# Kernel optimization log

Hardware: AMD Instinct MI355X
Metric: run time of the kernel (lower is better)

Reference implementation:

```python
import jax, jax.numpy as jnp
import numpy as np

A_COEF = 4e-4
B_COEF = 2e-2
T = 0.5
ATT = 1.0


def setup_inputs() -> dict:
    key = jax.random.key(0)
    k1, k2, k3, k4 = jax.random.split(key, 4)
    return {
        "targets": jnp.zeros((1,), dtype=jnp.int32),
        "stu1": jax.random.normal(k1, (8, 256, 64, 64), dtype=jnp.float32),
        "tea1": jax.random.normal(k2, (8, 256, 64, 64), dtype=jnp.float32),
        "stu2": jax.random.normal(k3, (8, 512, 32, 32), dtype=jnp.float32),
        "tea2": jax.random.normal(k4, (8, 512, 32, 32), dtype=jnp.float32),
    }


def _level_terms(s, t):
    # s, t: [B, C, H, W]
    BS, C, H, W = s.shape
    HW = H * W
    # spatial attention maps [B,H,W] and channel attention maps [B,C]
    Gs_s = jnp.abs(s).sum(axis=1) / C
    Gs_t = jnp.abs(t).sum(axis=1) / C
    Gc_s = jnp.abs(s).sum(axis=(2, 3)) / HW
    Gc_t = jnp.abs(t).sum(axis=(2, 3)) / HW
    # sum-reduction MSE between attention maps
    lat = jnp.sum((Gs_s - Gs_t) ** 2) + jnp.sum((Gc_s - Gc_t) ** 2)
    # spatial softmax mask over flattened HW (matches per-batch exp/max/sum loop)
    Ms = HW * jax.nn.softmax(((Gs_s + Gs_t) / T).reshape(BS, HW), axis=1).reshape(BS, H, W)
    # channel softmax mask
    Mc = C * jax.nn.softmax((Gc_s + Gc_t) / T, axis=1)
    # slam = sum_{b,c} Mc[b,c] * sum_{h,w} (s-t)^2 * Ms[b,h,w]
    slam = jnp.einsum('bchw,bhw,bc->', (s - t) ** 2, Ms, Mc)
    return lat, jnp.sqrt(slam)


def reference(targets, stu1, tea1, stu2, tea2):
    levels = ((stu1, tea1), (stu2, tea2))
    lat = jnp.float32(0.0)
    lam = jnp.float32(0.0)
    BS = stu1.shape[0]
    for s, t in levels:
        l_at, l_am = _level_terms(s, t)
        lat = lat + l_at
        lam = lam + l_am
    att_loss = ATT * (A_COEF * lat + B_COEF * lam) / BS / len(levels)
    return (att_loss * BS, jax.lax.stop_gradient(att_loss)[None])
```

## Files before the change

kernel.cpp:

```cpp
#include <hip/hip_runtime.h>
#include <hip/hip_fp16.h>
#include <math.h>

#define B_   8
#define C1   256
#define HW1  4096
#define C2   512
#define HW2  1024

#define CCH  8
#define HWT  1024
#define NCH1 32
#define NCH2 64
#define NT1  4
#define NT2  1

#define NB1  (B_*NT1*NCH1)
#define NB2  (B_*NCH2)
#define NBS  (NB1+NB2)

#define F_LATP  0
#define F_SL1P  (F_LATP + 32)
#define F_SL2P  (F_SL1P + NB1)
#define F_CP1S  (F_SL2P + NB2)
#define F_CP1T  (F_CP1S + B_*C1*NT1)
#define F_CP2S  (F_CP1T + B_*C1*NT1)
#define F_CP2T  (F_CP2S + B_*C2)
#define F_GS1S  (F_CP2T + B_*C2)
#define F_GS1T  (F_GS1S + B_*HW1)
#define F_GS2S  (F_GS1T + B_*HW1)
#define F_GS2T  (F_GS2S + B_*HW2)
#define F_MS1   (F_GS2T + B_*HW2)
#define F_MC1   (F_MS1 + B_*HW1)
#define F_MS2   (F_MC1 + B_*C1)
#define F_MC2   (F_MS2 + B_*HW2)
#define F_APH   (F_MC2 + B_*C2)
#define NH1     (NCH1*B_*HW1)
#define NH2     (NCH2*B_*HW2)
#define APH_FLOATS ((2*NH1 + 2*NH2) / 2)
#define F_D8    (F_APH + APH_FLOATS)
#define ND1     (B_*C1*HW1)
#define ND2     (B_*C2*HW2)

struct alignas(8) h4 { __half2 a, b; };
typedef float v2f __attribute__((ext_vector_type(2)));

__device__ __forceinline__ float wave_reduce_sum(float v) {
#pragma unroll
    for (int off = 1; off < 64; off <<= 1) v += __shfl_xor(v, off, 64);
    return v;
}
__device__ __forceinline__ float wave_reduce_max(float v) {
#pragma unroll
    for (int off = 1; off < 64; off <<= 1) v = fmaxf(v, __shfl_xor(v, off, 64));
    return v;
}
__device__ __forceinline__ float block_reduce_sum(float v, float* red) {
    const int lane = threadIdx.x & 63, wid = threadIdx.x >> 6;
    v = wave_reduce_sum(v);
    if (lane == 0) red[wid] = v;
    __syncthreads();
    v = red[0] + red[1] + red[2] + red[3];
    __syncthreads();
    return v;
}
__device__ __forceinline__ float block_reduce_max(float v, float* red) {
    const int lane = threadIdx.x & 63, wid = threadIdx.x >> 6;
    v = wave_reduce_max(v);
    if (lane == 0) red[wid] = v;
    __syncthreads();
    v = fmaxf(fmaxf(red[0], red[1]), fmaxf(red[2], red[3]));
    __syncthreads();
    return v;
}

__device__ __forceinline__ unsigned int pack4_fp8(float q0, float q1, float q2, float q3) {
    int u = 0;
    u = __builtin_amdgcn_cvt_pk_fp8_f32(q0, q1, u, false);
    u = __builtin_amdgcn_cvt_pk_fp8_f32(q2, q3, u, true);
    return (unsigned int)u;
}

template<int C, int HW, int NT>
__device__ void stats_level(const float* __restrict__ s, const float* __restrict__ t,
                            __half* __restrict__ APs, __half* __restrict__ APt,
                            float* __restrict__ CPs, float* __restrict__ CPt,
                            unsigned int* __restrict__ d8,
                            int b, int tile, int chunk, float (*part)[256]) {
    const int tid = threadIdx.x, lane = tid & 63, wid = tid >> 6;
    const int hw0 = tile * HWT + tid * 4;
    const int c0 = chunk * CCH;
    const size_t base = ((size_t)(b * C + c0)) * HW + hw0;
    const float4* ps = reinterpret_cast<const float4*>(s + base);
    const float4* pt = reinterpret_cast<const float4*>(t + base);
    unsigned int* dp = d8 + (((size_t)(b * C + c0)) * (HW / 4) + (hw0 >> 2));
    const int cstride = HW / 4;

    float as0 = 0.f, as1 = 0.f, as2 = 0.f, as3 = 0.f;
    float at0 = 0.f, at1 = 0.f, at2 = 0.f, at3 = 0.f;
    float css[CCH], cst[CCH];

#pragma unroll
    for (int ci = 0; ci < CCH; ++ci) {
        float4 vs = ps[(size_t)ci * cstride];
        float4 vt = pt[(size_t)ci * cstride];
        float a0 = fabsf(vs.x), a1 = fabsf(vs.y), a2 = fabsf(vs.z), a3 = fabsf(vs.w);
        float b0 = fabsf(vt.x), b1 = fabsf(vt.y), b2 = fabsf(vt.z), b3 = fabsf(vt.w);
        as0 += a0; as1 += a1; as2 += a2; as3 += a3;
        at0 += b0; at1 += b1; at2 += b2; at3 += b3;
        css[ci] = (a0 + a1) + (a2 + a3);
        cst[ci] = (b0 + b1) + (b2 + b3);
        const float d0 = vs.x - vt.x, d1 = vs.y - vt.y, d2 = vs.z - vt.z, d3 = vs.w - vt.w;
        dp[(size_t)ci * cstride] = pack4_fp8(d0 * d0, d1 * d1, d2 * d2, d3 * d3);
    }
    const size_t apH = ((size_t)chunk * B_ + b) * HW + hw0;
    h4 hs, ht;
    hs.a = __floats2half2_rn(as0, as1); hs.b = __floats2half2_rn(as2, as3);
    ht.a = __floats2half2_rn(at0, at1); ht.b = __floats2half2_rn(at2, at3);
    *reinterpret_cast<h4*>(APs + apH) = hs;
    *reinterpret_cast<h4*>(APt + apH) = ht;

#pragma unroll
    for (int ci = 0; ci < CCH; ++ci) {
        part[ci][tid] = css[ci];
        part[CCH + ci][tid] = cst[ci];
    }
    __syncthreads();
#pragma unroll
    for (int k = 0; k < 4; ++k) {
        const int r = wid * 4 + k;
        const float* cb = part[r];
        float v = (cb[lane] + cb[lane + 64]) + (cb[lane + 128] + cb[lane + 192]);
        v = wave_reduce_sum(v);
        if (lane == 0) {
            const int cc = r & (CCH - 1);
            float* dst = (r < CCH) ? CPs : CPt;
            dst[((size_t)b * C + c0 + cc) * NT + tile] = v;
        }
    }
}

__global__ __launch_bounds__(256) void stats_fast(const float* __restrict__ s1, const float* __restrict__ t1,
                                                  const float* __restrict__ s2, const float* __restrict__ t2,
                                                  float* ws) {
    __shared__ float part[2 * CCH][256];
    const int bid = blockIdx.x;
    __half* aph = reinterpret_cast<__half*>(ws + F_APH);
    unsigned int* d8 = reinterpret_cast<unsigned int*>(ws + F_D8);
    if (bid < NB1) {
        const int b = bid >> 7, rem = bid & 127, tile = rem >> 5, chunk = rem & 31;
        stats_level<C1, HW1, NT1>(s1, t1, aph, aph + NH1, ws + F_CP1S, ws + F_CP1T,
                                  d8, b, tile, chunk, part);
    } else {
        const int bid2 = bid - NB1;
        const int b = bid2 >> 6, chunk = bid2 & 63;
        stats_level<C2, HW2, NT2>(s2, t2, aph + 2 * NH1, aph + 2 * NH1 + NH2, ws + F_CP2S, ws + F_CP2T,
                                  d8 + ND1 / 4, b, 0, chunk, part);
    }
}

__global__ __launch_bounds__(256) void reduce_as(float* __restrict__ ws) {
    const int gid = blockIdx.x * 256 + threadIdx.x;
    const __half* aph = reinterpret_cast<const __half*>(ws + F_APH);
    if (gid < 2 * B_ * (HW1 / 4)) {
        const int tt = gid >> 13, rem = gid & 8191;
        const int b = rem >> 10, q = rem & 1023;
        const h4* src = reinterpret_cast<const h4*>(aph + (tt ? NH1 : 0))
                        + (size_t)b * (HW1 / 4) + q;
        float4 acc = make_float4(0.f, 0.f, 0.f, 0.f);
#pragma unroll
        for (int k = 0; k < NCH1; ++k) {
            const h4 v = src[(size_t)k * B_ * (HW1 / 4)];
            const float2 lo = __half22float2(v.a), hi = __half22float2(v.b);
            acc.x += lo.x; acc.y += lo.y; acc.z += hi.x; acc.w += hi.y;
        }
        reinterpret_cast<float4*>(ws + (tt ? F_GS1T : F_GS1S))[(size_t)b * (HW1 / 4) + q] = acc;
    } else {
        const int g2 = gid - 2 * B_ * (HW1 / 4);
        const int tt = g2 >> 11, rem = g2 & 2047;
        const int b = rem >> 8, q = rem & 255;
        const h4* src = reinterpret_cast<const h4*>(aph + 2 * NH1 + (tt ? NH2 : 0))
                        + (size_t)b * (HW2 / 4) + q;
        float4 acc = make_float4(0.f, 0.f, 0.f, 0.f);
#pragma unroll
        for (int k = 0; k < NCH2; ++k) {
            const h4 v = src[(size_t)k * B_ * (HW2 / 4)];
            const float2 lo = __half22float2(v.a), hi = __half22float2(v.b);
            acc.x += lo.x; acc.y += lo.y; acc.z += hi.x; acc.w += hi.y;
        }
        reinterpret_cast<float4*>(ws + (tt ? F_GS2T : F_GS2S))[(size_t)b * (HW2 / 4) + q] = acc;
    }
}

__global__ __launch_bounds__(256) void softmax_fast(float* ws) {
    __shared__ float sa[HW1], sb[HW1];
    __shared__ float red[4];
    const int bid = blockIdx.x;
    const int b = bid >> 2, m = bid & 3;
    const int tid = threadIdx.x;

    int n; float scale, mult; float* M;
    if (m == 0)      { n = HW1; scale = 1.0f / C1;  mult = (float)HW1; M = ws + F_MS1 + b * HW1; }
    else if (m == 1) { n = C1;  scale = 1.0f / HW1; mult = (float)C1;  M = ws + F_MC1 + b * C1;  }
    else if (m == 2) { n = HW2; scale = 1.0f / C2;  mult = (float)HW2; M = ws + F_MS2 + b * HW2; }
    else             { n = C2;  scale = 1.0f / HW2; mult = (float)C2;  M = ws + F_MC2 + b * C2;  }

    if (m == 0) {
        const float* As = ws + F_GS1S + b * HW1;
        const float* At = ws + F_GS1T + b * HW1;
        for (int i = tid; i < HW1; i += 256) { sa[i] = As[i] * scale; sb[i] = At[i] * scale; }
    } else if (m == 1) {
        if (tid < C1) {
            float4 v = *reinterpret_cast<const float4*>(ws + F_CP1S + ((size_t)b * C1 + tid) * 4);
            float4 w = *reinterpret_cast<const float4*>(ws + F_CP1T + ((size_t)b * C1 + tid) * 4);
            sa[tid] = ((v.x + v.y) + (v.z + v.w)) * scale;
            sb[tid] = ((w.x + w.y) + (w.z + w.w)) * scale;
        }
    } else if (m == 2) {
        const float* As = ws + F_GS2S + b * HW2;
        const float* At = ws + F_GS2T + b * HW2;
        for (int i = tid; i < HW2; i += 256) { sa[i] = As[i] * scale; sb[i] = At[i] * scale; }
    } else {
        for (int i = tid; i < C2; i += 256) {
            sa[i] = ws[F_CP2S + b * C2 + i] * scale;
            sb[i] = ws[F_CP2T + b * C2 + i] * scale;
        }
    }
    __syncthreads();

    const float invT = 2.0f;
    float latp = 0.f, mx = -3.0e38f;
    for (int i = tid; i < n; i += 256) {
        float d = sa[i] - sb[i];
        latp += d * d;
        mx = fmaxf(mx, (sa[i] + sb[i]) * invT);
    }
    const float mxall = block_reduce_max(mx, red);
    const float latall = block_reduce_sum(latp, red);
    if (tid == 0) ws[F_LATP + bid] = latall;

    float se = 0.f;
    for (int i = tid; i < n; i += 256) se += expf((sa[i] + sb[i]) * invT - mxall);
    const float seall = block_reduce_sum(se, red);
    const float inv = mult / seall;
    for (int i = tid; i < n; i += 256)
        M[i] = expf((sa[i] + sb[i]) * invT - mxall) * inv;
}

template<int C, int HW>
__device__ float slam_level(const unsigned int* __restrict__ d8,
                            const float* Ms, const float* Mc,
                            int b, int tile, int chunk, float* mc, float* red) {
    const int tid = threadIdx.x;
    const int hw0 = tile * HWT + tid * 4;
    const int c0 = chunk * CCH;
    if (tid < CCH) mc[tid] = Mc[b * C + c0 + tid];
    __syncthreads();
    const unsigned int* dp = d8 + (((size_t)(b * C + c0)) * (HW / 4) + (hw0 >> 2));
    const int cstride = HW / 4;

    float a0 = 0.f, a1 = 0.f, a2 = 0.f, a3 = 0.f;
#pragma unroll
    for (int ci = 0; ci < CCH; ++ci) {
        const int u = (int)dp[(size_t)ci * cstride];
        const float m = mc[ci];
        const v2f lo = __builtin_amdgcn_cvt_pk_f32_fp8(u, false);
        const v2f hi = __builtin_amdgcn_cvt_pk_f32_fp8(u, true);
        a0 = fmaf(m, lo.x, a0);
        a1 = fmaf(m, lo.y, a1);
        a2 = fmaf(m, hi.x, a2);
        a3 = fmaf(m, hi.y, a3);
    }
    const float4 msv = *reinterpret_cast<const float4*>(Ms + b * HW + hw0);
    float acc = a0 * msv.x + a1 * msv.y + a2 * msv.z + a3 * msv.w;
    return block_reduce_sum(acc, red);
}

__global__ __launch_bounds__(256) void slam_d2(float* __restrict__ ws) {
    __shared__ float mc[CCH];
    __shared__ float red[4];
    const int bid = blockIdx.x;
    const unsigned int* d8 = reinterpret_cast<const unsigned int*>(ws + F_D8);

    if (bid < NB1) {
        const int b = bid >> 7, rem = bid & 127, tile = rem >> 5, chunk = rem & 31;
        float acc = slam_level<C1, HW1>(d8, ws + F_MS1, ws + F_MC1, b, tile, chunk, mc, red);
        if (threadIdx.x == 0) ws[F_SL1P + bid] = acc;
    } else {
        const int bid2 = bid - NB1;
        const int b = bid2 >> 6, chunk = bid2 & 63;
        float acc = slam_level<C2, HW2>(d8 + ND1 / 4, ws + F_MS2, ws + F_MC2, b, 0, chunk, mc, red);
        if (threadIdx.x == 0) ws[F_SL2P + bid2] = acc;
    }
}

__global__ __launch_bounds__(256) void final_fast(const float* __restrict__ ws, float* __restrict__ out) {
    __shared__ float red[4];
    const int tid = threadIdx.x;
    float lat = 0.f, p1 = 0.f, p2 = 0.f;
    for (int i = tid; i < 32; i += 256)   lat += ws[F_LATP + i];
    for (int i = tid; i < NB1; i += 256)  p1 += ws[F_SL1P + i];
    for (int i = tid; i < NB2; i += 256)  p2 += ws[F_SL2P + i];
    lat = block_reduce_sum(lat, red);
    p1 = block_reduce_sum(p1, red);
    p2 = block_reduce_sum(p2, red);
    if (tid == 0) {
        const float lam = sqrtf(p1) + sqrtf(p2);
        const float att = (4e-4f * lat + 2e-2f * lam) / 16.0f;
        out[0] = att * 8.0f;
        out[1] = att;
    }
}


extern "C" void kernel_launch(void* const* d_in, const int* in_sizes, int n_in,
                              void* d_out, int out_size, void* d_ws, size_t ws_size,
                              hipStream_t stream) {
    (void)in_sizes; (void)n_in; (void)out_size; (void)ws_size;
    const float* s1 = (const float*)d_in[1];
    const float* t1 = (const float*)d_in[2];
    const float* s2 = (const float*)d_in[3];
    const float* t2 = (const float*)d_in[4];
    float* ws = (float*)d_ws;
    float* out = (float*)d_out;

    stats_fast<<<NBS, 256, 0, stream>>>(s1, t1, s2, t2, ws);
    reduce_as<<<80, 256, 0, stream>>>(ws);
    softmax_fast<<<32, 256, 0, stream>>>(ws);
    slam_d2<<<NBS, 256, 0, stream>>>(ws);
    final_fast<<<1, 256, 0, stream>>>(ws, out);
}
```

Baseline: 42.76 us.

## Store fp8 diffs per-thread contiguous and interleave student/teacher partial attention

Changes the intermediate workspace layout. Each thread's eight packed fp8 squared-difference words now sit together, so they are written and read back as two 16-byte vector accesses. Student and teacher half-precision spatial partial sums are interleaved into one 16-byte record, which halves the reduce_as thread count because each thread handles both. The aim is fewer, wider memory transactions between stats and slam. The cost is that the per-thread layout ties the stats and slam kernels to the same block/thread mapping.

```diff
diff --git a/kernel.cpp b/kernel.cpp
--- a/kernel.cpp
+++ b/kernel.cpp
@@ -35,14 +35,14 @@
 #define F_MS2   (F_MC1 + B_*C1)
 #define F_MC2   (F_MS2 + B_*HW2)
 #define F_APH   (F_MC2 + B_*C2)
-#define NH1     (NCH1*B_*HW1)
-#define NH2     (NCH2*B_*HW2)
-#define APH_FLOATS ((2*NH1 + 2*NH2) / 2)
+#define NP1     (NCH1*B_*(HW1/4))
+#define NP2     (NCH2*B_*(HW2/4))
+#define APH_FLOATS ((NP1 + NP2) * 4)
 #define F_D8    (F_APH + APH_FLOATS)
-#define ND1     (B_*C1*HW1)
-#define ND2     (B_*C2*HW2)
-
-struct alignas(8) h4 { __half2 a, b; };
+#define ND1U    (NB1*256*8)
+#define ND2U    (NB2*256*8)
+
+struct alignas(16) h8 { __half2 sa, sb, ta, tb; };
 typedef float v2f __attribute__((ext_vector_type(2)));
 
 __device__ __forceinline__ float wave_reduce_sum(float v) {
@@ -83,9 +83,9 @@
 
 template<int C, int HW, int NT>
 __device__ void stats_level(const float* __restrict__ s, const float* __restrict__ t,
-                            __half* __restrict__ APs, __half* __restrict__ APt,
+                            h8* __restrict__ AP,
                             float* __restrict__ CPs, float* __restrict__ CPt,
-                            unsigned int* __restrict__ d8,
+                            unsigned int* __restrict__ dthr,
                             int b, int tile, int chunk, float (*part)[256]) {
     const int tid = threadIdx.x, lane = tid & 63, wid = tid >> 6;
     const int hw0 = tile * HWT + tid * 4;
@@ -93,12 +93,12 @@
     const size_t base = ((size_t)(b * C + c0)) * HW + hw0;
     const float4* ps = reinterpret_cast<const float4*>(s + base);
     const float4* pt = reinterpret_cast<const float4*>(t + base);
-    unsigned int* dp = d8 + (((size_t)(b * C + c0)) * (HW / 4) + (hw0 >> 2));
     const int cstride = HW / 4;
 
     float as0 = 0.f, as1 = 0.f, as2 = 0.f, as3 = 0.f;
     float at0 = 0.f, at1 = 0.f, at2 = 0.f, at3 = 0.f;
     float css[CCH], cst[CCH];
+    unsigned int pk8[CCH];
 
 #pragma unroll
     for (int ci = 0; ci < CCH; ++ci) {
@@ -111,14 +111,15 @@
         css[ci] = (a0 + a1) + (a2 + a3);
         cst[ci] = (b0 + b1) + (b2 + b3);
         const float d0 = vs.x - vt.x, d1 = vs.y - vt.y, d2 = vs.z - vt.z, d3 = vs.w - vt.w;
-        dp[(size_t)ci * cstride] = pack4_fp8(d0 * d0, d1 * d1, d2 * d2, d3 * d3);
-    }
-    const size_t apH = ((size_t)chunk * B_ + b) * HW + hw0;
-    h4 hs, ht;
-    hs.a = __floats2half2_rn(as0, as1); hs.b = __floats2half2_rn(as2, as3);
-    ht.a = __floats2half2_rn(at0, at1); ht.b = __floats2half2_rn(at2, at3);
-    *reinterpret_cast<h4*>(APs + apH) = hs;
-    *reinterpret_cast<h4*>(APt + apH) = ht;
+        pk8[ci] = pack4_fp8(d0 * d0, d1 * d1, d2 * d2, d3 * d3);
+    }
+    *reinterpret_cast<uint4*>(dthr)     = make_uint4(pk8[0], pk8[1], pk8[2], pk8[3]);
+    *reinterpret_cast<uint4*>(dthr + 4) = make_uint4(pk8[4], pk8[5], pk8[6], pk8[7]);
+
+    h8 rec;
+    rec.sa = __floats2half2_rn(as0, as1); rec.sb = __floats2half2_rn(as2, as3);
+    rec.ta = __floats2half2_rn(at0, at1); rec.tb = __floats2half2_rn(at2, at3);
+    AP[((size_t)chunk * B_ + b) * (HW / 4) + (hw0 >> 2)] = rec;
 
 #pragma unroll
     for (int ci = 0; ci < CCH; ++ci) {
@@ -144,51 +145,55 @@
                                                   const float* __restrict__ s2, const float* __restrict__ t2,
                                                   float* ws) {
     __shared__ float part[2 * CCH][256];
-    const int bid = blockIdx.x;
-    __half* aph = reinterpret_cast<__half*>(ws + F_APH);
+    const int bid = blockIdx.x, tid = threadIdx.x;
+    h8* ap = reinterpret_cast<h8*>(ws + F_APH);
     unsigned int* d8 = reinterpret_cast<unsigned int*>(ws + F_D8);
     if (bid < NB1) {
         const int b = bid >> 7, rem = bid & 127, tile = rem >> 5, chunk = rem & 31;
-        stats_level<C1, HW1, NT1>(s1, t1, aph, aph + NH1, ws + F_CP1S, ws + F_CP1T,
-                                  d8, b, tile, chunk, part);
+        unsigned int* dthr = d8 + ((size_t)bid * 256 + tid) * 8;
+        stats_level<C1, HW1, NT1>(s1, t1, ap, ws + F_CP1S, ws + F_CP1T, dthr, b, tile, chunk, part);
     } else {
         const int bid2 = bid - NB1;
         const int b = bid2 >> 6, chunk = bid2 & 63;
-        stats_level<C2, HW2, NT2>(s2, t2, aph + 2 * NH1, aph + 2 * NH1 + NH2, ws + F_CP2S, ws + F_CP2T,
-                                  d8 + ND1 / 4, b, 0, chunk, part);
+        unsigned int* dthr = d8 + ND1U + ((size_t)bid2 * 256 + tid) * 8;
+        stats_level<C2, HW2, NT2>(s2, t2, ap + NP1, ws + F_CP2S, ws + F_CP2T, dthr, b, 0, chunk, part);
     }
 }
 
 __global__ __launch_bounds__(256) void reduce_as(float* __restrict__ ws) {
     const int gid = blockIdx.x * 256 + threadIdx.x;
-    const __half* aph = reinterpret_cast<const __half*>(ws + F_APH);
-    if (gid < 2 * B_ * (HW1 / 4)) {
-        const int tt = gid >> 13, rem = gid & 8191;
-        const int b = rem >> 10, q = rem & 1023;
-        const h4* src = reinterpret_cast<const h4*>(aph + (tt ? NH1 : 0))
-                        + (size_t)b * (HW1 / 4) + q;
-        float4 acc = make_float4(0.f, 0.f, 0.f, 0.f);
+    const h8* ap = reinterpret_cast<const h8*>(ws + F_APH);
+    if (gid < B_ * (HW1 / 4)) {
+        const int b = gid >> 10, q = gid & 1023;
+        const h8* src = ap + (size_t)b * (HW1 / 4) + q;
+        float4 aS = make_float4(0.f, 0.f, 0.f, 0.f);
+        float4 aT = make_float4(0.f, 0.f, 0.f, 0.f);
 #pragma unroll
         for (int k = 0; k < NCH1; ++k) {
-            const h4 v = src[(size_t)k * B_ * (HW1 / 4)];
-            const float2 lo = __half22float2(v.a), hi = __half22float2(v.b);
-            acc.x += lo.x; acc.y += lo.y; acc.z += hi.x; acc.w += hi.y;
-        }
-        reinterpret_cast<float4*>(ws + (tt ? F_GS1T : F_GS1S))[(size_t)b * (HW1 / 4) + q] = acc;
-    } else {
-        const int g2 = gid - 2 * B_ * (HW1 / 4);
-        const int tt = g2 >> 11, rem = g2 & 2047;
-        const int b = rem >> 8, q = rem & 255;
-        const h4* src = reinterpret_cast<const h4*>(aph + 2 * NH1 + (tt ? NH2 : 0))
-                        + (size_t)b * (HW2 / 4) + q;
-        float4 acc = make_float4(0.f, 0.f, 0.f, 0.f);
+            const h8 v = src[(size_t)k * B_ * (HW1 / 4)];
+            const float2 s0 = __half22float2(v.sa), s1 = __half22float2(v.sb);
+            const float2 t0 = __half22float2(v.ta), t1 = __half22float2(v.tb);
+            aS.x += s0.x; aS.y += s0.y; aS.z += s1.x; aS.w += s1.y;
+            aT.x += t0.x; aT.y += t0.y; aT.z += t1.x; aT.w += t1.y;
+        }
+        reinterpret_cast<float4*>(ws + F_GS1S)[(size_t)b * (HW1 / 4) + q] = aS;
+        reinterpret_cast<float4*>(ws + F_GS1T)[(size_t)b * (HW1 / 4) + q] = aT;
+    } else if (gid < B_ * (HW1 / 4) + B_ * (HW2 / 4)) {
+        const int g2 = gid - B_ * (HW1 / 4);
+        const int b = g2 >> 8, q = g2 & 255;
+        const h8* src = ap + NP1 + (size_t)b * (HW2 / 4) + q;
+        float4 aS = make_float4(0.f, 0.f, 0.f, 0.f);
+        float4 aT = make_float4(0.f, 0.f, 0.f, 0.f);
 #pragma unroll
         for (int k = 0; k < NCH2; ++k) {
-            const h4 v = src[(size_t)k * B_ * (HW2 / 4)];
-            const float2 lo = __half22float2(v.a), hi = __half22float2(v.b);
-            acc.x += lo.x; acc.y += lo.y; acc.z += hi.x; acc.w += hi.y;
-        }
-        reinterpret_cast<float4*>(ws + (tt ? F_GS2T : F_GS2S))[(size_t)b * (HW2 / 4) + q] = acc;
+            const h8 v = src[(size_t)k * B_ * (HW2 / 4)];
+            const float2 s0 = __half22float2(v.sa), s1 = __half22float2(v.sb);
+            const float2 t0 = __half22float2(v.ta), t1 = __half22float2(v.tb);
+            aS.x += s0.x; aS.y += s0.y; aS.z += s1.x; aS.w += s1.y;
+            aT.x += t0.x; aT.y += t0.y; aT.z += t1.x; aT.w += t1.y;
+        }
+        reinterpret_cast<float4*>(ws + F_GS2S)[(size_t)b * (HW2 / 4) + q] = aS;
+        reinterpret_cast<float4*>(ws + F_GS2T)[(size_t)b * (HW2 / 4) + q] = aT;
     }
 }
 
@@ -248,7 +253,7 @@
 }
 
 template<int C, int HW>
-__device__ float slam_level(const unsigned int* __restrict__ d8,
+__device__ float slam_level(const unsigned int* __restrict__ dthr,
                             const float* Ms, const float* Mc,
                             int b, int tile, int chunk, float* mc, float* red) {
     const int tid = threadIdx.x;
@@ -256,13 +261,15 @@
     const int c0 = chunk * CCH;
     if (tid < CCH) mc[tid] = Mc[b * C + c0 + tid];
     __syncthreads();
-    const unsigned int* dp = d8 + (((size_t)(b * C + c0)) * (HW / 4) + (hw0 >> 2));
-    const int cstride = HW / 4;
+
+    const uint4 u0 = *reinterpret_cast<const uint4*>(dthr);
+    const uint4 u1 = *reinterpret_cast<const uint4*>(dthr + 4);
+    unsigned int pk8[CCH] = {u0.x, u0.y, u0.z, u0.w, u1.x, u1.y, u1.z, u1.w};
 
     float a0 = 0.f, a1 = 0.f, a2 = 0.f, a3 = 0.f;
 #pragma unroll
     for (int ci = 0; ci < CCH; ++ci) {
-        const int u = (int)dp[(size_t)ci * cstride];
+        const int u = (int)pk8[ci];
         const float m = mc[ci];
         const v2f lo = __builtin_amdgcn_cvt_pk_f32_fp8(u, false);
         const v2f hi = __builtin_amdgcn_cvt_pk_f32_fp8(u, true);
@@ -279,18 +286,20 @@
 __global__ __launch_bounds__(256) void slam_d2(float* __restrict__ ws) {
     __shared__ float mc[CCH];
     __shared__ float red[4];
-    const int bid = blockIdx.x;
+    const int bid = blockIdx.x, tid = threadIdx.x;
     const unsigned int* d8 = reinterpret_cast<const unsigned int*>(ws + F_D8);
 
     if (bid < NB1) {
         const int b = bid >> 7, rem = bid & 127, tile = rem >> 5, chunk = rem & 31;
-        float acc = slam_level<C1, HW1>(d8, ws + F_MS1, ws + F_MC1, b, tile, chunk, mc, red);
-        if (threadIdx.x == 0) ws[F_SL1P + bid] = acc;
+        const unsigned int* dthr = d8 + ((size_t)bid * 256 + tid) * 8;
+        float acc = slam_level<C1, HW1>(dthr, ws + F_MS1, ws + F_MC1, b, tile, chunk, mc, red);
+        if (tid == 0) ws[F_SL1P + bid] = acc;
     } else {
         const int bid2 = bid - NB1;
         const int b = bid2 >> 6, chunk = bid2 & 63;
-        float acc = slam_level<C2, HW2>(d8 + ND1 / 4, ws + F_MS2, ws + F_MC2, b, 0, chunk, mc, red);
-        if (threadIdx.x == 0) ws[F_SL2P + bid2] = acc;
+        const unsigned int* dthr = d8 + ND1U + ((size_t)bid2 * 256 + tid) * 8;
+        float acc = slam_level<C2, HW2>(dthr, ws + F_MS2, ws + F_MC2, b, 0, chunk, mc, red);
+        if (tid == 0) ws[F_SL2P + bid2] = acc;
     }
 }
 
@@ -325,7 +334,7 @@
     float* out = (float*)d_out;
 
     stats_fast<<<NBS, 256, 0, stream>>>(s1, t1, s2, t2, ws);
-    reduce_as<<<80, 256, 0, stream>>>(ws);
+    reduce_as<<<40, 256, 0, stream>>>(ws);
     softmax_fast<<<32, 256, 0, stream>>>(ws);
     slam_d2<<<NBS, 256, 0, stream>>>(ws);
     final_fast<<<1, 256, 0, stream>>>(ws, out);
```

Measured after the change: 59.25 us. 1.39x slower.
